# Optimization experiments

Hardware: AMD Instinct MI355X
Metric: run time of the kernel (lower is better)

## Reference

```python
import jax, jax.numpy as jnp
import numpy as np

EPS_KERNEL = 1e-4   # softmax_kernel eps
EPS_DENOM = 1e-6    # causal linear attention denominator eps
CHUNK = 128


def _gaussian_orthogonal(nb_rows, nb_cols, rng):
    # Matches gaussian_orthogonal_random_matrix with scaling=0
    blocks = []
    n_full = nb_rows // nb_cols
    for _ in range(n_full):
        g = rng.standard_normal((nb_cols, nb_cols))
        qm, _ = np.linalg.qr(g)
        blocks.append(qm.T)
    rem = nb_rows - n_full * nb_cols
    if rem > 0:
        g = rng.standard_normal((nb_cols, nb_cols))
        qm, _ = np.linalg.qr(g)
        blocks.append(qm.T[:rem])
    mat = np.concatenate(blocks, axis=0)
    mult = np.linalg.norm(rng.standard_normal((nb_rows, nb_cols)), axis=1)
    return (mult[:, None] * mat).astype(np.float32)


def setup_inputs() -> dict:
    key = jax.random.key(0)
    k1, k2, k3 = jax.random.split(key, 3)
    b, h, n, d, m = 2, 8, 4096, 64, 256
    q = jax.random.normal(k1, (b, h, n, d), jnp.float32)
    k = jax.random.normal(k2, (b, h, n, d), jnp.float32)
    v = jax.random.normal(k3, (b, h, n, d), jnp.float32)
    proj = jnp.asarray(_gaussian_orthogonal(m, d, np.random.default_rng(0)))
    return {"q": q, "k": k, "v": v, "proj": proj}


def _softmax_kernel(data, proj, is_query):
    # FAVOR+ positive random features (softmax_kernel in the torch source)
    d = data.shape[-1]
    normalizer = d ** -0.25
    ratio = proj.shape[0] ** -0.5
    # [b,h,n,m]
    dd = jnp.einsum('bhid,jd->bhij', normalizer * data, proj)
    diag = (jnp.sum(data * data, axis=-1) * 0.5 * normalizer ** 2)[..., None]
    if is_query:
        mx = jax.lax.stop_gradient(jnp.max(dd, axis=-1, keepdims=True))
    else:
        mx = jax.lax.stop_gradient(jnp.max(dd, axis=(-1, -2), keepdims=True))
    return ratio * (jnp.exp(dd - diag - mx) + EPS_KERNEL)


def _causal_linear_attention(q, k, v):
    # Chunked-recurrent exact causal linear attention:
    # out_n = q_n . (sum_{m<=n} k_m v_m^T) / (q_n . (sum_{m<=n} k_m + eps))
    b, h, n, m = q.shape
    e = v.shape[-1]
    nc = n // CHUNK
    qc = q.reshape(b, h, nc, CHUNK, m).transpose(2, 0, 1, 3, 4)
    kc = k.reshape(b, h, nc, CHUNK, m).transpose(2, 0, 1, 3, 4)
    vc = v.reshape(b, h, nc, CHUNK, e).transpose(2, 0, 1, 3, 4)
    mask = jnp.tril(jnp.ones((CHUNK, CHUNK), dtype=bool))

    def step(carry, blk):
        S, z = carry          # S: [b,h,m,e] running k v^T sum; z: [b,h,m] running k sum
        qb, kb, vb = blk      # [b,h,C,m], [b,h,C,m], [b,h,C,e]
        z_cum = z[:, :, None, :] + jnp.cumsum(kb, axis=2)          # [b,h,C,m]
        denom = jnp.einsum('bhcm,bhcm->bhc', qb, z_cum + EPS_DENOM)
        inter = jnp.einsum('bhcm,bhme->bhce', qb, S)               # past chunks
        scores = jnp.einsum('bhcm,bhdm->bhcd', qb, kb)             # within chunk
        scores = jnp.where(mask, scores, 0.0)
        intra = jnp.einsum('bhcd,bhde->bhce', scores, vb)
        out = (inter + intra) / denom[..., None]
        S = S + jnp.einsum('bhcm,bhce->bhme', kb, vb)
        return (S, z_cum[:, :, -1, :]), out

    S0 = jnp.zeros((b, h, m, e), q.dtype)
    z0 = jnp.zeros((b, h, m), q.dtype)
    _, outs = jax.lax.scan(step, (S0, z0), (qc, kc, vc))           # [nc,b,h,C,e]
    return outs.transpose(1, 2, 0, 3, 4).reshape(b, h, n, e)


def reference(q, k, v, proj):
    phi_q = _softmax_kernel(q, proj, is_query=True)
    phi_k = _softmax_kernel(k, proj, is_query=False)
    return _causal_linear_attention(phi_q, phi_k, v)
```

## Files before the change

kernel.cpp:

```cpp
#include <hip/hip_runtime.h>


constexpr int kBH = 16;
constexpr int kN  = 4096;
constexpr int kD  = 64;
constexpr int kM  = 256;
constexpr int kE  = 64;
constexpr int kC  = 128;
constexpr int kNC = 32;
constexpr float kNorm  = 0.35355339059327373f;
constexpr float kDiagC = 0.0625f;
constexpr float kRatio = 0.0625f;
constexpr float kEpsK  = 1e-4f;
constexpr float kEpsD  = 1e-6f;

typedef short s8v __attribute__((ext_vector_type(8)));
typedef float f4v __attribute__((ext_vector_type(4)));

__device__ __forceinline__ float dec_max(unsigned u) {
  unsigned b = (u & 0x80000000u) ? (u & 0x7fffffffu) : ~u;
  return __uint_as_float(b);
}
__device__ __forceinline__ unsigned short f2bf(float x) {
  unsigned u = __float_as_uint(x);
  return (unsigned short)((u + 0x7FFFu + ((u >> 16) & 1u)) >> 16);
}
__device__ __forceinline__ float bf2f(unsigned short b) {
  return __uint_as_float(((unsigned)b) << 16);
}

template <bool IS_Q>
__global__ __launch_bounds__(256, 3) void k_proj(const float* __restrict__ data,
                                                 const float* __restrict__ proj,
                                                 float* __restrict__ outv,
                                                 unsigned* __restrict__ kmaxU) {
  __shared__ __align__(16) float dT[16][68];
  __shared__ __align__(16) float pT[16][260];
  __shared__ float diagL[64];
  __shared__ float wmaxL[4];

  const int t = threadIdx.x;
  const int j = t & 63;
  const int w = t >> 6;
  const int r0 = 16 * w;
  const long row0 = (long)blockIdx.x * 64;

  {
    const int r = t >> 2, off = (t & 3) * 16;
    const float* dp = data + (row0 + r) * kD + off;
    float ss = 0.f;
#pragma unroll
    for (int u = 0; u < 4; ++u) {
      float4 dv = *reinterpret_cast<const float4*>(dp + 4 * u);
      ss = fmaf(dv.x, dv.x, ss); ss = fmaf(dv.y, dv.y, ss);
      ss = fmaf(dv.z, dv.z, ss); ss = fmaf(dv.w, dv.w, ss);
    }
    ss += __shfl_xor(ss, 1);
    ss += __shfl_xor(ss, 2);
    if ((t & 3) == 0) diagL[r] = ss * kDiagC;
  }

  float acc[16][4];
#pragma unroll
  for (int i = 0; i < 16; ++i)
#pragma unroll
    for (int u = 0; u < 4; ++u) acc[i][u] = 0.f;

  for (int kt = 0; kt < 4; ++kt) {
    __syncthreads();
    {
      const int row = t >> 2, k4 = (t & 3) * 4;
      float4 dv = *reinterpret_cast<const float4*>(
          &data[(row0 + row) * kD + kt * 16 + k4]);
      dT[k4 + 0][row] = dv.x; dT[k4 + 1][row] = dv.y;
      dT[k4 + 2][row] = dv.z; dT[k4 + 3][row] = dv.w;
    }
#pragma unroll
    for (int i = 0; i < 4; ++i) {
      const int flat = i * 256 + t;
      const int m = flat >> 2, k4 = (flat & 3) * 4;
      float4 pv = *reinterpret_cast<const float4*>(
          &proj[(long)m * kD + kt * 16 + k4]);
      pT[k4 + 0][m] = pv.x; pT[k4 + 1][m] = pv.y;
      pT[k4 + 2][m] = pv.z; pT[k4 + 3][m] = pv.w;
    }
    __syncthreads();

#pragma unroll 4
    for (int kk = 0; kk < 16; ++kk) {
      float4 b = *reinterpret_cast<const float4*>(&pT[kk][4 * j]);
      float a[16];
#pragma unroll
      for (int g = 0; g < 4; ++g) {
        float4 av = *reinterpret_cast<const float4*>(&dT[kk][r0 + 4 * g]);
        a[4 * g + 0] = av.x; a[4 * g + 1] = av.y;
        a[4 * g + 2] = av.z; a[4 * g + 3] = av.w;
      }
#pragma unroll
      for (int i = 0; i < 16; ++i) {
        acc[i][0] = fmaf(a[i], b.x, acc[i][0]);
        acc[i][1] = fmaf(a[i], b.y, acc[i][1]);
        acc[i][2] = fmaf(a[i], b.z, acc[i][2]);
        acc[i][3] = fmaf(a[i], b.w, acc[i][3]);
      }
    }
  }

#pragma unroll
  for (int i = 0; i < 16; ++i)
#pragma unroll
    for (int u = 0; u < 4; ++u) acc[i][u] *= kNorm;

  if (IS_Q) {
#pragma unroll
    for (int i = 0; i < 16; ++i) {
      float m2 = fmaxf(fmaxf(acc[i][0], acc[i][1]), fmaxf(acc[i][2], acc[i][3]));
      m2 = fmaxf(m2, __shfl_xor(m2, 1));
      m2 = fmaxf(m2, __shfl_xor(m2, 2));
      m2 = fmaxf(m2, __shfl_xor(m2, 4));
      m2 = fmaxf(m2, __shfl_xor(m2, 8));
      m2 = fmaxf(m2, __shfl_xor(m2, 16));
      m2 = fmaxf(m2, __shfl_xor(m2, 32));
      const float dg = diagL[r0 + i];
      float4 o;
      o.x = kRatio * (__expf(acc[i][0] - dg - m2) + kEpsK);
      o.y = kRatio * (__expf(acc[i][1] - dg - m2) + kEpsK);
      o.z = kRatio * (__expf(acc[i][2] - dg - m2) + kEpsK);
      o.w = kRatio * (__expf(acc[i][3] - dg - m2) + kEpsK);
      *reinterpret_cast<float4*>(&outv[(row0 + r0 + i) * kM + 4 * j]) = o;
    }
  } else {
    float bm = -3.0e38f;
#pragma unroll
    for (int i = 0; i < 16; ++i) {
      const float dg = diagL[r0 + i];
      bm = fmaxf(bm, fmaxf(fmaxf(acc[i][0], acc[i][1]),
                           fmaxf(acc[i][2], acc[i][3])));
      float4 o;
      o.x = __expf(acc[i][0] - dg); o.y = __expf(acc[i][1] - dg);
      o.z = __expf(acc[i][2] - dg); o.w = __expf(acc[i][3] - dg);
      *reinterpret_cast<float4*>(&outv[(row0 + r0 + i) * kM + 4 * j]) = o;
    }
    bm = fmaxf(bm, __shfl_xor(bm, 1));
    bm = fmaxf(bm, __shfl_xor(bm, 2));
    bm = fmaxf(bm, __shfl_xor(bm, 4));
    bm = fmaxf(bm, __shfl_xor(bm, 8));
    bm = fmaxf(bm, __shfl_xor(bm, 16));
    bm = fmaxf(bm, __shfl_xor(bm, 32));
    if ((t & 63) == 0) wmaxL[w] = bm;
    __syncthreads();
    if (t == 0) {
      float b2 = fmaxf(fmaxf(wmaxL[0], wmaxL[1]), fmaxf(wmaxL[2], wmaxL[3]));
      unsigned ub = __float_as_uint(b2);
      ub = (ub & 0x80000000u) ? ~ub : (ub | 0x80000000u);
      atomicMax(kmaxU + (int)(row0 >> 12), ub);
    }
  }
}

__device__ __forceinline__ int phi_col(int m) { return m + 4 * ((m >> 4) & 7); }

__global__ __launch_bounds__(256, 2) void k_chunk(const float* __restrict__ Eb,
                                                  const float* __restrict__ v,
                                                  const unsigned* __restrict__ kmaxU,
                                                  float* __restrict__ Sc,
                                                  float* __restrict__ zc) {
  __shared__ __align__(16) float phE[16][284];
  __shared__ __align__(16) float vT[16][68];

  const int t = threadIdx.x;
  const int bh = blockIdx.x >> 5;
  const int c = blockIdx.x & 31;
  const float sR = kRatio * __expf(-dec_max(kmaxU[bh]));
  const float epsR = kRatio * kEpsK;
  const long rowbase = (long)bh * kN + (long)c * kC;
  const float* Ep = Eb + rowbase * kM;
  const float* vp = v + rowbase * kE;

  const int et = t & 15, mg = t >> 4;
  const int e0 = 4 * et, m0 = 16 * mg;
  const int pcol = phi_col(m0);

  float acc[16][4];
#pragma unroll
  for (int i = 0; i < 16; ++i)
#pragma unroll
    for (int u = 0; u < 4; ++u) acc[i][u] = 0.f;
  float zsum = 0.f;

  for (int rt = 0; rt < 8; ++rt) {
    __syncthreads();
#pragma unroll
    for (int i = 0; i < 4; ++i) {
      const int flat = i * 256 + t;
      const int rr = flat >> 6;
      const int m4 = (flat & 63) * 4;
      float4 xx = *reinterpret_cast<const float4*>(
          &Ep[(long)(rt * 16 + rr) * kM + m4]);
      float4 ph;
      ph.x = fmaf(xx.x, sR, epsR);
      ph.y = fmaf(xx.y, sR, epsR);
      ph.z = fmaf(xx.z, sR, epsR);
      ph.w = fmaf(xx.w, sR, epsR);
      *reinterpret_cast<float4*>(&phE[rr][phi_col(m4)]) = ph;
    }
    {
      const int rr = t >> 4, ee = (t & 15) * 4;
      float4 vv = *reinterpret_cast<const float4*>(
          &vp[(long)(rt * 16 + rr) * kE + ee]);
      *reinterpret_cast<float4*>(&vT[rr][ee]) = vv;
    }
    __syncthreads();

    for (int r = 0; r < 16; ++r) {
      float4 bv = *reinterpret_cast<const float4*>(&vT[r][e0]);
      float pv[16];
#pragma unroll
      for (int a = 0; a < 4; ++a) {
        float4 p4 = *reinterpret_cast<const float4*>(&phE[r][pcol + 4 * a]);
        pv[4 * a + 0] = p4.x; pv[4 * a + 1] = p4.y;
        pv[4 * a + 2] = p4.z; pv[4 * a + 3] = p4.w;
      }
#pragma unroll
      for (int i = 0; i < 16; ++i) {
        acc[i][0] = fmaf(pv[i], bv.x, acc[i][0]);
        acc[i][1] = fmaf(pv[i], bv.y, acc[i][1]);
        acc[i][2] = fmaf(pv[i], bv.z, acc[i][2]);
        acc[i][3] = fmaf(pv[i], bv.w, acc[i][3]);
      }
    }
    {
      const int zcol = phi_col(t);
      float zp = 0.f;
#pragma unroll
      for (int r = 0; r < 16; ++r) zp += phE[r][zcol];
      zsum += zp;
    }
  }

  float* scp = Sc + (long)(bh * kNC + c) * (kM * kE);
#pragma unroll
  for (int i = 0; i < 16; ++i) {
    float4 o = make_float4(acc[i][0], acc[i][1], acc[i][2], acc[i][3]);
    *reinterpret_cast<float4*>(&scp[(long)(m0 + i) * kE + e0]) = o;
  }
  zc[(long)(bh * kNC + c) * kM + t] = zsum;
}

__global__ __launch_bounds__(256) void k_prefix(float* __restrict__ Sc,
                                                float* __restrict__ zc) {
  const int bid = blockIdx.x;
  if (bid < 256) {
    const int bh = bid >> 4;
    const int f4 = (bid & 15) * 256 + threadIdx.x;
    float4* base = reinterpret_cast<float4*>(Sc) + (long)bh * kNC * 4096 + f4;
    float4 run = make_float4(0.f, 0.f, 0.f, 0.f);
#pragma unroll 4
    for (int c = 0; c < kNC; ++c) {
      float4 tmp = base[(long)c * 4096];
      base[(long)c * 4096] = run;
      run.x += tmp.x; run.y += tmp.y; run.z += tmp.z; run.w += tmp.w;
    }
  } else {
    const int bh = bid - 256;
    const int m = threadIdx.x;
    long base = (long)bh * kNC * kM + m;
    float run = 0.f;
    for (int c = 0; c < kNC; ++c) {
      float tmp = zc[base + (long)c * kM];
      zc[base + (long)c * kM] = run;
      run += tmp;
    }
  }
}

constexpr int kPadAB = 40;
constexpr int kPadSC = 69;
constexpr int kPadIT = 68;

struct PA_t {
  unsigned short Aqh[128][kPadAB], Aql[128][kPadAB];
  unsigned short Bkh[128][kPadAB], Bkl[128][kPadAB];
  unsigned short Sh[80][kPadAB], Sl[80][kPadAB];
};
struct PB_t {
  float sc[kC][kPadSC];
  float inter[kC][kPadIT];
  float den[kC];
};
union SmemV { PA_t a; PB_t b; };

__global__ __launch_bounds__(256, 2) void k_out(const float* __restrict__ phiq,
                                                const float* __restrict__ Eb,
                                                const float* __restrict__ v,
                                                const float* __restrict__ Sc,
                                                const float* __restrict__ zc,
                                                const unsigned* __restrict__ kmaxU,
                                                float* __restrict__ outp) {
  __shared__ __align__(16) SmemV sm;

  const int t = threadIdx.x;
  const int l15 = t & 15;
  const int g = (t >> 4) & 3;
  const int w = t >> 6;
  const int rbase = w * 32;
  const int bh = blockIdx.x >> 5;
  const int c = blockIdx.x & 31;
  const float mx = dec_max(kmaxU[bh]);
  const float sR = kRatio * __expf(-mx);
  const float epsR = kRatio * kEpsK;

  const long row0 = (long)bh * kN + (long)c * kC;
  const float* phiq_p = phiq + row0 * kM;
  const float* E_p = Eb + row0 * kM;
  const float* v_p = v + row0 * kE;
  const float* S_p = Sc + (long)(bh * kNC + c) * (kM * kE);
  const float* z_p = zc + (long)(bh * kNC + c) * kM;

  for (int idx = t; idx < 480; idx += 256) {
    const int r = 65 + (idx >> 5), m = idx & 31;
    sm.a.Sh[r][m] = 0; sm.a.Sl[r][m] = 0;
  }

  f4v accS[2][8];
  f4v accI[2][5];
#pragma unroll
  for (int rt = 0; rt < 2; ++rt) {
#pragma unroll
    for (int ct = 0; ct < 8; ++ct) accS[rt][ct] = (f4v){0.f, 0.f, 0.f, 0.f};
#pragma unroll
    for (int et = 0; et < 5; ++et) accI[rt][et] = (f4v){0.f, 0.f, 0.f, 0.f};
  }

  for (int mt = 0; mt < 8; ++mt) {
    __syncthreads();
#pragma unroll
    for (int i = 0; i < 4; ++i) {
      const int f = i * 256 + t;
      const int row = f >> 3, mq = (f & 7) * 4;
      float4 xq = *reinterpret_cast<const float4*>(&phiq_p[(long)row * kM + mt * 32 + mq]);
      ushort4 h, lo;
      h.x = f2bf(xq.x); lo.x = f2bf(xq.x - bf2f(h.x));
      h.y = f2bf(xq.y); lo.y = f2bf(xq.y - bf2f(h.y));
      h.z = f2bf(xq.z); lo.z = f2bf(xq.z - bf2f(h.z));
      h.w = f2bf(xq.w); lo.w = f2bf(xq.w - bf2f(h.w));
      *reinterpret_cast<ushort4*>(&sm.a.Aqh[row][mq]) = h;
      *reinterpret_cast<ushort4*>(&sm.a.Aql[row][mq]) = lo;
      float4 xe = *reinterpret_cast<const float4*>(&E_p[(long)row * kM + mt * 32 + mq]);
      float4 pk;
      pk.x = fmaf(xe.x, sR, epsR); pk.y = fmaf(xe.y, sR, epsR);
      pk.z = fmaf(xe.z, sR, epsR); pk.w = fmaf(xe.w, sR, epsR);
      h.x = f2bf(pk.x); lo.x = f2bf(pk.x - bf2f(h.x));
      h.y = f2bf(pk.y); lo.y = f2bf(pk.y - bf2f(h.y));
      h.z = f2bf(pk.z); lo.z = f2bf(pk.z - bf2f(h.z));
      h.w = f2bf(pk.w); lo.w = f2bf(pk.w - bf2f(h.w));
      *reinterpret_cast<ushort4*>(&sm.a.Bkh[row][mq]) = h;
      *reinterpret_cast<ushort4*>(&sm.a.Bkl[row][mq]) = lo;
    }
#pragma unroll
    for (int i = 0; i < 2; ++i) {
      const int f = i * 256 + t;
      const int ml = f >> 4, e4 = (f & 15) * 4;
      float4 sv = *reinterpret_cast<const float4*>(&S_p[(long)(mt * 32 + ml) * kE + e4]);
      unsigned short hh;
      hh = f2bf(sv.x); sm.a.Sh[e4 + 0][ml] = hh; sm.a.Sl[e4 + 0][ml] = f2bf(sv.x - bf2f(hh));
      hh = f2bf(sv.y); sm.a.Sh[e4 + 1][ml] = hh; sm.a.Sl[e4 + 1][ml] = f2bf(sv.y - bf2f(hh));
      hh = f2bf(sv.z); sm.a.Sh[e4 + 2][ml] = hh; sm.a.Sl[e4 + 2][ml] = f2bf(sv.z - bf2f(hh));
      hh = f2bf(sv.w); sm.a.Sh[e4 + 3][ml] = hh; sm.a.Sl[e4 + 3][ml] = f2bf(sv.w - bf2f(hh));
    }
    if (t < 32) {
      float zez = z_p[mt * 32 + t] + kEpsD;
      unsigned short hh = f2bf(zez);
      sm.a.Sh[64][t] = hh; sm.a.Sl[64][t] = f2bf(zez - bf2f(hh));
    }
    __syncthreads();

    s8v aqh[2], aql[2];
#pragma unroll
    for (int rt = 0; rt < 2; ++rt) {
      aqh[rt] = *reinterpret_cast<const s8v*>(&sm.a.Aqh[rbase + rt * 16 + l15][g * 8]);
      aql[rt] = *reinterpret_cast<const s8v*>(&sm.a.Aql[rbase + rt * 16 + l15][g * 8]);
    }
#pragma unroll
    for (int ct = 0; ct < 8; ++ct) {
      s8v bh_ = *reinterpret_cast<const s8v*>(&sm.a.Bkh[ct * 16 + l15][g * 8]);
      s8v bl_ = *reinterpret_cast<const s8v*>(&sm.a.Bkl[ct * 16 + l15][g * 8]);
#pragma unroll
      for (int rt = 0; rt < 2; ++rt) {
        accS[rt][ct] = __builtin_amdgcn_mfma_f32_16x16x32_bf16(aqh[rt], bh_, accS[rt][ct], 0, 0, 0);
        accS[rt][ct] = __builtin_amdgcn_mfma_f32_16x16x32_bf16(aqh[rt], bl_, accS[rt][ct], 0, 0, 0);
        accS[rt][ct] = __builtin_amdgcn_mfma_f32_16x16x32_bf16(aql[rt], bh_, accS[rt][ct], 0, 0, 0);
      }
    }
#pragma unroll
    for (int et = 0; et < 5; ++et) {
      s8v sh_ = *reinterpret_cast<const s8v*>(&sm.a.Sh[et * 16 + l15][g * 8]);
      s8v sl_ = *reinterpret_cast<const s8v*>(&sm.a.Sl[et * 16 + l15][g * 8]);
#pragma unroll
      for (int rt = 0; rt < 2; ++rt) {
        accI[rt][et] = __builtin_amdgcn_mfma_f32_16x16x32_bf16(aqh[rt], sh_, accI[rt][et], 0, 0, 0);
        accI[rt][et] = __builtin_amdgcn_mfma_f32_16x16x32_bf16(aqh[rt], sl_, accI[rt][et], 0, 0, 0);
        accI[rt][et] = __builtin_amdgcn_mfma_f32_16x16x32_bf16(aql[rt], sh_, accI[rt][et], 0, 0, 0);
      }
    }
  }
  __syncthreads();

#pragma unroll
  for (int rt = 0; rt < 2; ++rt) {
#pragma unroll
    for (int et = 0; et < 4; ++et) {
      f4v vv = accI[rt][et];
#pragma unroll
      for (int reg = 0; reg < 4; ++reg)
        sm.b.inter[rbase + rt * 16 + g * 4 + reg][et * 16 + l15] = vv[reg];
    }
    if (l15 == 0) {
      f4v dv = accI[rt][4];
#pragma unroll
      for (int reg = 0; reg < 4; ++reg)
        sm.b.den[rbase + rt * 16 + g * 4 + reg] = dv[reg];
    }
  }

  const int tr = t >> 4;
  const int tc = t & 15;
  const int r0 = tr * 8;
  const int e0 = tc * 4;

  float intra_[8][4];
  float denb[8];
#pragma unroll
  for (int i = 0; i < 8; ++i) {
    denb[i] = 0.f;
#pragma unroll
    for (int jj = 0; jj < 4; ++jj) intra_[i][jj] = 0.f;
  }

#pragma unroll
  for (int half = 0; half < 2; ++half) {
    __syncthreads();
#pragma unroll
    for (int cti = 0; cti < 4; ++cti) {
      const int ct = half * 4 + cti;
#pragma unroll
      for (int rt = 0; rt < 2; ++rt) {
        f4v vv = accS[rt][ct];
#pragma unroll
        for (int reg = 0; reg < 4; ++reg) {
          const int r = rbase + rt * 16 + g * 4 + reg;
          const int cg = ct * 16 + l15;
          sm.b.sc[r][cti * 16 + l15] = (cg <= r) ? vv[reg] : 0.f;
        }
      }
    }
    __syncthreads();
    const float* vh = v_p + (long)half * 64 * kE;
    for (int k2 = 0; k2 < 64; ++k2) {
      float as[8];
#pragma unroll
      for (int i = 0; i < 8; ++i) as[i] = sm.b.sc[r0 + i][k2];
      const float4 vv = *reinterpret_cast<const float4*>(vh + (long)k2 * kE + e0);
#pragma unroll
      for (int i = 0; i < 8; ++i) {
        denb[i] += as[i];
        intra_[i][0] = fmaf(as[i], vv.x, intra_[i][0]);
        intra_[i][1] = fmaf(as[i], vv.y, intra_[i][1]);
        intra_[i][2] = fmaf(as[i], vv.z, intra_[i][2]);
        intra_[i][3] = fmaf(as[i], vv.w, intra_[i][3]);
      }
    }
  }

  float* op = outp + row0 * kE;
#pragma unroll
  for (int i = 0; i < 8; ++i) {
    const float4 itv = *reinterpret_cast<const float4*>(&sm.b.inter[r0 + i][e0]);
    const float dinv = 1.0f / (sm.b.den[r0 + i] + denb[i]);
    float4 o;
    o.x = (itv.x + intra_[i][0]) * dinv;
    o.y = (itv.y + intra_[i][1]) * dinv;
    o.z = (itv.z + intra_[i][2]) * dinv;
    o.w = (itv.w + intra_[i][3]) * dinv;
    *reinterpret_cast<float4*>(op + (long)(r0 + i) * kE + e0) = o;
  }
}

extern "C" void kernel_launch(void* const* d_in, const int* in_sizes, int n_in,
                              void* d_out, int out_size, void* d_ws, size_t ws_size,
                              hipStream_t stream) {
  const float* q = (const float*)d_in[0];
  const float* k = (const float*)d_in[1];
  const float* v = (const float*)d_in[2];
  const float* proj = (const float*)d_in[3];
  float* out = (float*)d_out;
  float* ws = (float*)d_ws;

  float* phiq = ws;
  float* Eb = ws + 16777216L;
  float* Sc = ws + 33554432L;
  float* zc = ws + 41943040L;
  unsigned* kmaxU = (unsigned*)(ws + 42074112L);

  hipMemsetAsync(kmaxU, 0, kBH * sizeof(unsigned), stream);
  k_proj<true><<<dim3(1024), dim3(256), 0, stream>>>(q, proj, phiq, nullptr);
  k_proj<false><<<dim3(1024), dim3(256), 0, stream>>>(k, proj, Eb, kmaxU);
  k_chunk<<<dim3(512), dim3(256), 0, stream>>>(Eb, v, kmaxU, Sc, zc);
  k_prefix<<<dim3(272), dim3(256), 0, stream>>>(Sc, zc);
  k_out<<<dim3(512), dim3(256), 0, stream>>>(phiq, Eb, v, Sc, zc, kmaxU, out);
}
```

Measured before the change: 263.8 us.

## Compute intra-chunk scores×V with split-bf16 MFMA instead of scalar FMA

Replaces the scalar fp32 FMA loop for the masked intra-chunk scores times V product with split-bf16 (hi/lo) MFMA instructions. The masked scores and a transposed V tile are staged in shared memory in four k-steps, and the results accumulate directly into the existing inter-chunk accumulators. The intra-chunk denominator row sums are now taken from registers with a cross-lane shuffle reduction instead of the scalar loop. This trades ALU-bound work for MFMA work at the cost of extra conversions, more barriers and a small precision loss from dropping the lo×lo term.

```diff
diff --git a/kernel.cpp b/kernel.cpp
--- a/kernel.cpp
+++ b/kernel.cpp
@@ -275,8 +275,6 @@
 }
 
 constexpr int kPadAB = 40;
-constexpr int kPadSC = 69;
-constexpr int kPadIT = 68;
 
 struct PA_t {
   unsigned short Aqh[128][kPadAB], Aql[128][kPadAB];
@@ -284,11 +282,14 @@
   unsigned short Sh[80][kPadAB], Sl[80][kPadAB];
 };
 struct PB_t {
-  float sc[kC][kPadSC];
-  float inter[kC][kPadIT];
-  float den[kC];
+  unsigned short Ah[128][kPadAB], Al[128][kPadAB];
+  unsigned short vTh[64][kPadAB], vTl[64][kPadAB];
 };
-union SmemV { PA_t a; PB_t b; };
+struct PC_t {
+  float outF[128][68];
+  float den[128];
+};
+union SmemV { PA_t a; PB_t b; PC_t c; };
 
 __global__ __launch_bounds__(256, 2) void k_out(const float* __restrict__ phiq,
                                                 const float* __restrict__ Eb,
@@ -404,7 +405,83 @@
       }
     }
   }
+
+  float denb[2][4];
+#pragma unroll
+  for (int rt = 0; rt < 2; ++rt) {
+#pragma unroll
+    for (int reg = 0; reg < 4; ++reg) denb[rt][reg] = 0.f;
+#pragma unroll
+    for (int ct = 0; ct < 8; ++ct) {
+      f4v vv = accS[rt][ct];
+#pragma unroll
+      for (int reg = 0; reg < 4; ++reg) {
+        const int row = rbase + rt * 16 + g * 4 + reg;
+        const int col = ct * 16 + l15;
+        denb[rt][reg] += (col <= row) ? vv[reg] : 0.f;
+      }
+    }
+#pragma unroll
+    for (int reg = 0; reg < 4; ++reg) {
+      float s = denb[rt][reg];
+      s += __shfl_xor(s, 1);
+      s += __shfl_xor(s, 2);
+      s += __shfl_xor(s, 4);
+      s += __shfl_xor(s, 8);
+      denb[rt][reg] = s;
+    }
+  }
+
   __syncthreads();
+
+#pragma unroll
+  for (int ks = 0; ks < 4; ++ks) {
+#pragma unroll
+    for (int i = 0; i < 2; ++i) {
+      const int r = i * 16 + (t >> 4);
+      const int e4 = (t & 15) * 4;
+      float4 vv = *reinterpret_cast<const float4*>(
+          &v_p[(long)(ks * 32 + r) * kE + e4]);
+      unsigned short hh;
+      hh = f2bf(vv.x); sm.b.vTh[e4 + 0][r] = hh; sm.b.vTl[e4 + 0][r] = f2bf(vv.x - bf2f(hh));
+      hh = f2bf(vv.y); sm.b.vTh[e4 + 1][r] = hh; sm.b.vTl[e4 + 1][r] = f2bf(vv.y - bf2f(hh));
+      hh = f2bf(vv.z); sm.b.vTh[e4 + 2][r] = hh; sm.b.vTl[e4 + 2][r] = f2bf(vv.z - bf2f(hh));
+      hh = f2bf(vv.w); sm.b.vTh[e4 + 3][r] = hh; sm.b.vTl[e4 + 3][r] = f2bf(vv.w - bf2f(hh));
+    }
+#pragma unroll
+    for (int cti = 0; cti < 2; ++cti) {
+      const int ct = ks * 2 + cti;
+#pragma unroll
+      for (int rt = 0; rt < 2; ++rt) {
+        f4v vv = accS[rt][ct];
+#pragma unroll
+        for (int reg = 0; reg < 4; ++reg) {
+          const int row = rbase + rt * 16 + g * 4 + reg;
+          const int col = ct * 16 + l15;
+          const float x = (col <= row) ? vv[reg] : 0.f;
+          const unsigned short hh = f2bf(x);
+          sm.b.Ah[row][cti * 16 + l15] = hh;
+          sm.b.Al[row][cti * 16 + l15] = f2bf(x - bf2f(hh));
+        }
+      }
+    }
+    __syncthreads();
+
+#pragma unroll
+    for (int rt = 0; rt < 2; ++rt) {
+      s8v ah = *reinterpret_cast<const s8v*>(&sm.b.Ah[rbase + rt * 16 + l15][g * 8]);
+      s8v al = *reinterpret_cast<const s8v*>(&sm.b.Al[rbase + rt * 16 + l15][g * 8]);
+#pragma unroll
+      for (int et = 0; et < 4; ++et) {
+        s8v bh_ = *reinterpret_cast<const s8v*>(&sm.b.vTh[et * 16 + l15][g * 8]);
+        s8v bl_ = *reinterpret_cast<const s8v*>(&sm.b.vTl[et * 16 + l15][g * 8]);
+        accI[rt][et] = __builtin_amdgcn_mfma_f32_16x16x32_bf16(ah, bh_, accI[rt][et], 0, 0, 0);
+        accI[rt][et] = __builtin_amdgcn_mfma_f32_16x16x32_bf16(ah, bl_, accI[rt][et], 0, 0, 0);
+        accI[rt][et] = __builtin_amdgcn_mfma_f32_16x16x32_bf16(al, bh_, accI[rt][et], 0, 0, 0);
+      }
+    }
+    __syncthreads();
+  }
 
 #pragma unroll
   for (int rt = 0; rt < 2; ++rt) {
@@ -413,75 +490,29 @@
       f4v vv = accI[rt][et];
 #pragma unroll
       for (int reg = 0; reg < 4; ++reg)
-        sm.b.inter[rbase + rt * 16 + g * 4 + reg][et * 16 + l15] = vv[reg];
+        sm.c.outF[rbase + rt * 16 + g * 4 + reg][et * 16 + l15] = vv[reg];
     }
     if (l15 == 0) {
       f4v dv = accI[rt][4];
 #pragma unroll
       for (int reg = 0; reg < 4; ++reg)
-        sm.b.den[rbase + rt * 16 + g * 4 + reg] = dv[reg];
-    }
-  }
+        sm.c.den[rbase + rt * 16 + g * 4 + reg] = dv[reg] + denb[rt][reg];
+    }
+  }
+  __syncthreads();
 
   const int tr = t >> 4;
   const int tc = t & 15;
   const int r0 = tr * 8;
   const int e0 = tc * 4;
-
-  float intra_[8][4];
-  float denb[8];
+  float* op = outp + row0 * kE;
 #pragma unroll
   for (int i = 0; i < 8; ++i) {
-    denb[i] = 0.f;
-#pragma unroll
-    for (int jj = 0; jj < 4; ++jj) intra_[i][jj] = 0.f;
-  }
-
-#pragma unroll
-  for (int half = 0; half < 2; ++half) {
-    __syncthreads();
-#pragma unroll
-    for (int cti = 0; cti < 4; ++cti) {
-      const int ct = half * 4 + cti;
-#pragma unroll
-      for (int rt = 0; rt < 2; ++rt) {
-        f4v vv = accS[rt][ct];
-#pragma unroll
-        for (int reg = 0; reg < 4; ++reg) {
-          const int r = rbase + rt * 16 + g * 4 + reg;
-          const int cg = ct * 16 + l15;
-          sm.b.sc[r][cti * 16 + l15] = (cg <= r) ? vv[reg] : 0.f;
-        }
-      }
-    }
-    __syncthreads();
-    const float* vh = v_p + (long)half * 64 * kE;
-    for (int k2 = 0; k2 < 64; ++k2) {
-      float as[8];
-#pragma unroll
-      for (int i = 0; i < 8; ++i) as[i] = sm.b.sc[r0 + i][k2];
-      const float4 vv = *reinterpret_cast<const float4*>(vh + (long)k2 * kE + e0);
-#pragma unroll
-      for (int i = 0; i < 8; ++i) {
-        denb[i] += as[i];
-        intra_[i][0] = fmaf(as[i], vv.x, intra_[i][0]);
-        intra_[i][1] = fmaf(as[i], vv.y, intra_[i][1]);
-        intra_[i][2] = fmaf(as[i], vv.z, intra_[i][2]);
-        intra_[i][3] = fmaf(as[i], vv.w, intra_[i][3]);
-      }
-    }
-  }
-
-  float* op = outp + row0 * kE;
-#pragma unroll
-  for (int i = 0; i < 8; ++i) {
-    const float4 itv = *reinterpret_cast<const float4*>(&sm.b.inter[r0 + i][e0]);
-    const float dinv = 1.0f / (sm.b.den[r0 + i] + denb[i]);
+    const float4 ov = *reinterpret_cast<const float4*>(&sm.c.outF[r0 + i][e0]);
+    const float dinv = 1.0f / sm.c.den[r0 + i];
     float4 o;
-    o.x = (itv.x + intra_[i][0]) * dinv;
-    o.y = (itv.y + intra_[i][1]) * dinv;
-    o.z = (itv.z + intra_[i][2]) * dinv;
-    o.w = (itv.w + intra_[i][3]) * dinv;
+    o.x = ov.x * dinv; o.y = ov.y * dinv;
+    o.z = ov.z * dinv; o.w = ov.w * dinv;
     *reinterpret_cast<float4*>(op + (long)(r0 + i) * kE + e0) = o;
   }
 }
```

After: 266.0 us. No clear change (+0.8%).
